# Optimization experiments

Measured on AMD Instinct MI355X. Metric: run time of the kernel, lower is better.

## Reference

```python
import jax, jax.numpy as jnp
import numpy as np

N_NODES = 100000
N_EDGES = 1250000
D_IN = 64
D_H = 64
D_OUT = 32


def setup_inputs() -> dict:
    key = jax.random.key(0)
    ks = jax.random.split(key, 8)
    x = jax.random.normal(ks[0], (N_NODES, D_IN), dtype=jnp.float32)
    edge_index = jax.random.randint(ks[1], (2, N_EDGES), 0, N_NODES, dtype=jnp.int64)
    s = 0.1
    W1_l = jax.random.normal(ks[2], (D_H, D_IN), dtype=jnp.float32) * s
    W1_r = jax.random.normal(ks[3], (D_H, D_IN), dtype=jnp.float32) * s
    b1 = jnp.zeros((D_H,), dtype=jnp.float32)
    W2_l = jax.random.normal(ks[4], (D_OUT, D_H), dtype=jnp.float32) * s
    W2_r = jax.random.normal(ks[5], (D_OUT, D_H), dtype=jnp.float32) * s
    b2 = jnp.zeros((D_OUT,), dtype=jnp.float32)
    return {"x": x, "edge_index": edge_index, "W1_l": W1_l, "W1_r": W1_r,
            "b1": b1, "W2_l": W2_l, "W2_r": W2_r, "b2": b2}


def _sage_conv(x, src, dst, W_l, W_r, b):
    # PyG SAGEConv (aggr='mean', root_weight=True):
    #   out = lin_l(mean_{j in N(i)} x_j) + lin_r(x_i)
    n = x.shape[0]
    msg = x[src]                                            # [E, d] gather
    ssum = jax.ops.segment_sum(msg, dst, num_segments=n)    # [N, d]
    deg = jax.ops.segment_sum(jnp.ones((src.shape[0], 1), x.dtype), dst,
                              num_segments=n)               # [N, 1]
    mean = ssum / jnp.maximum(deg, 1.0)
    return mean @ W_l.T + b + x @ W_r.T


def reference(x, edge_index, W1_l, W1_r, b1, W2_l, W2_r, b2):
    src = edge_index[0]
    dst = edge_index[1]
    h = jax.nn.relu(_sage_conv(x, src, dst, W1_l, W1_r, b1))
    out = _sage_conv(h, src, dst, W2_l, W2_r, b2)
    return out
```

## Files before the change

kernel.cpp:

```cpp
#include <hip/hip_runtime.h>

#define N_NODES 100000
#define N_EDGES 1250000
#define D_IN 64
#define D_H 64
#define D_OUT 32

#define BUCKETS 196
#define GRP 512
#define PREP_NB 512
#define PREP_CH 2442
#define SCAP 48
#define BSTRIDE (PREP_NB*SCAP)
#define CSRCAP 8192

typedef __attribute__((ext_vector_type(8))) short bf16x8;
typedef __attribute__((ext_vector_type(4))) float f32x4;

__device__ __forceinline__ unsigned short f2bf(float f) {
    unsigned u = __float_as_uint(f);
    u = (u + 0x7fffu + ((u >> 16) & 1u)) >> 16;
    return (unsigned short)u;
}
__device__ __forceinline__ float bfhi(unsigned v) { return __uint_as_float(v & 0xffff0000u); }
__device__ __forceinline__ float bflo(unsigned v) { return __uint_as_float(v << 16); }


__global__ __launch_bounds__(256) void k_prep(const float* __restrict__ x,
                                              unsigned short* __restrict__ xh,
                                              const int* __restrict__ src,
                                              const int* __restrict__ dst,
                                              int* __restrict__ ebuf,
                                              int* __restrict__ pcnt) {
    __shared__ int ofs[BUCKETS];
    int t = threadIdx.x, b = blockIdx.x;
    for (int i = t; i < BUCKETS; i += 256) ofs[i] = 0;
    __syncthreads();

    const int TOT = N_NODES * 64 / 4;
    for (int i = b * 256 + t; i < TOT; i += PREP_NB * 256) {
        float4 v = *(const float4*)(x + (size_t)i * 4);
        uint2 u;
        u.x = (unsigned)f2bf(v.x) | ((unsigned)f2bf(v.y) << 16);
        u.y = (unsigned)f2bf(v.z) | ((unsigned)f2bf(v.w) << 16);
        *(uint2*)(xh + (size_t)i * 4) = u;
    }

    int e0 = b * PREP_CH;
    int e1 = e0 + PREP_CH; if (e1 > N_EDGES) e1 = N_EDGES;
    for (int e = e0 + t; e < e1; e += 256) {
        int s = src[e], d = dst[e];
        if ((unsigned)d >= N_NODES) continue;
        int sv = ((unsigned)s < N_NODES) ? s : 0;
        int bk = d >> 9;
        int r = atomicAdd(&ofs[bk], 1);
        if (r < SCAP) ebuf[bk * BSTRIDE + b * SCAP + r] = ((d & 511) << 17) | sv;
    }
    __syncthreads();
    for (int i = t; i < BUCKETS; i += 256) {
        int v = ofs[i]; if (v > SCAP) v = SCAP;
        pcnt[b * BUCKETS + i] = v;
    }
}

__global__ __launch_bounds__(256) void k_phb(const int* __restrict__ ebuf,
                                             const int* __restrict__ pcnt,
                                             int2* __restrict__ rd,
                                             int* __restrict__ csr_src) {
    __shared__ int sedge[CSRCAP];
    __shared__ int pc[PREP_NB];
    __shared__ int cnt[GRP];
    __shared__ int part[256];
    int b = blockIdx.x, t = threadIdx.x;

    int c0 = pcnt[(2 * t) * BUCKETS + b];
    int c1 = pcnt[(2 * t + 1) * BUCKETS + b];
    int s = c0 + c1;
    part[t] = s;
    __syncthreads();
    for (int off = 1; off < 256; off <<= 1) {
        int u = (t >= off) ? part[t - off] : 0;
        __syncthreads();
        part[t] += u;
        __syncthreads();
    }
    int run = part[t] - s;
    pc[2 * t] = run;
    pc[2 * t + 1] = run + c0;
    int n = part[255]; if (n > CSRCAP) n = CSRCAP;
    for (int i = t; i < GRP; i += 256) cnt[i] = 0;
    {
        const int* sp = ebuf + b * BSTRIDE + (2 * t) * SCAP;
        int base = pc[2 * t];
        for (int j = 0; j < c0; ++j) if (base + j < CSRCAP) sedge[base + j] = sp[j];
        sp += SCAP;
        base = pc[2 * t + 1];
        for (int j = 0; j < c1; ++j) if (base + j < CSRCAP) sedge[base + j] = sp[j];
    }
    __syncthreads();
    for (int i = t; i < n; i += 256) atomicAdd(&cnt[sedge[i] >> 17], 1);
    __syncthreads();
    int d0 = cnt[2 * t], d1 = cnt[2 * t + 1];
    int s2 = d0 + d1;
    part[t] = s2;
    __syncthreads();
    for (int off = 1; off < 256; off <<= 1) {
        int u = (t >= off) ? part[t - off] : 0;
        __syncthreads();
        part[t] += u;
        __syncthreads();
    }
    int g0 = b * CSRCAP + part[t] - s2;
    int node0 = b * GRP + 2 * t;
    if (node0 + 1 < N_NODES) {
        *(int4*)(rd + node0) = make_int4(g0, d0, g0 + d0, d1);
    } else if (node0 < N_NODES) {
        rd[node0] = make_int2(g0, d0);
    }
    __syncthreads();
    cnt[2 * t] = g0;
    cnt[2 * t + 1] = g0 + d0;
    __syncthreads();
    for (int i = t; i < n; i += 256) {
        int v = sedge[i];
        int pos = atomicAdd(&cnt[v >> 17], 1);
        csr_src[pos] = v & 0x1FFFF;
    }
}

__global__ __launch_bounds__(256) void k_gather1(
    const unsigned short* __restrict__ xh,
    const int2* __restrict__ rd,
    const int* __restrict__ csr_src,
    unsigned int* __restrict__ meanh)
{
    int lane = threadIdx.x & 63;
    int wv = threadIdx.x >> 6;
    int c = lane & 31;
    int hb = lane & 32;
    const unsigned* xp = (const unsigned*)xh;

    int node0 = blockIdx.x * 8 + wv * 2 + (hb >> 5);
    for (int row = node0; row < N_NODES; row += gridDim.x * 8) {
        int2 rdv = rd[row];
        int start = rdv.x, dg = rdv.y;
        int end = start + dg;
        float x0 = 0.f, y0 = 0.f, x1 = 0.f, y1 = 0.f;
        float x2 = 0.f, y2 = 0.f, x3 = 0.f, y3 = 0.f;
        float x4 = 0.f, y4 = 0.f, x5 = 0.f, y5 = 0.f;
        float x6 = 0.f, y6 = 0.f, x7 = 0.f, y7 = 0.f;
        for (int eb = start; eb < end; eb += 32) {
            int nv = end - eb; if (nv > 32) nv = 32;
            int sid = (c < nv) ? csr_src[eb + c] : 0;
            int j = 0;
            for (; j + 8 <= nv; j += 8) {
                int s0 = __shfl(sid, hb + j + 0, 64);
                int s1 = __shfl(sid, hb + j + 1, 64);
                int s2 = __shfl(sid, hb + j + 2, 64);
                int s3 = __shfl(sid, hb + j + 3, 64);
                int s4 = __shfl(sid, hb + j + 4, 64);
                int s5 = __shfl(sid, hb + j + 5, 64);
                int s6 = __shfl(sid, hb + j + 6, 64);
                int s7 = __shfl(sid, hb + j + 7, 64);
                unsigned v0 = xp[s0 * 32 + c];
                unsigned v1 = xp[s1 * 32 + c];
                unsigned v2 = xp[s2 * 32 + c];
                unsigned v3 = xp[s3 * 32 + c];
                unsigned v4 = xp[s4 * 32 + c];
                unsigned v5 = xp[s5 * 32 + c];
                unsigned v6 = xp[s6 * 32 + c];
                unsigned v7 = xp[s7 * 32 + c];
                x0 += bflo(v0); y0 += bfhi(v0);
                x1 += bflo(v1); y1 += bfhi(v1);
                x2 += bflo(v2); y2 += bfhi(v2);
                x3 += bflo(v3); y3 += bfhi(v3);
                x4 += bflo(v4); y4 += bfhi(v4);
                x5 += bflo(v5); y5 += bfhi(v5);
                x6 += bflo(v6); y6 += bfhi(v6);
                x7 += bflo(v7); y7 += bfhi(v7);
            }
            for (; j + 4 <= nv; j += 4) {
                int s0 = __shfl(sid, hb + j + 0, 64);
                int s1 = __shfl(sid, hb + j + 1, 64);
                int s2 = __shfl(sid, hb + j + 2, 64);
                int s3 = __shfl(sid, hb + j + 3, 64);
                unsigned v0 = xp[s0 * 32 + c];
                unsigned v1 = xp[s1 * 32 + c];
                unsigned v2 = xp[s2 * 32 + c];
                unsigned v3 = xp[s3 * 32 + c];
                x0 += bflo(v0); y0 += bfhi(v0);
                x1 += bflo(v1); y1 += bfhi(v1);
                x2 += bflo(v2); y2 += bfhi(v2);
                x3 += bflo(v3); y3 += bfhi(v3);
            }
            for (; j < nv; ++j) {
                int s = __shfl(sid, hb + j, 64);
                unsigned v = xp[s * 32 + c];
                x0 += bflo(v); y0 += bfhi(v);
            }
        }
        float rdeg = 1.0f / fmaxf((float)dg, 1.0f);
        float fx = (((x0 + x1) + (x2 + x3)) + ((x4 + x5) + (x6 + x7))) * rdeg;
        float fy = (((y0 + y1) + (y2 + y3)) + ((y4 + y5) + (y6 + y7))) * rdeg;
        meanh[(size_t)row * 32 + c] = (unsigned)f2bf(fx) | ((unsigned)f2bf(fy) << 16);
    }
}

__global__ __launch_bounds__(256) void k_gemm1(
    const unsigned short* __restrict__ xh, const unsigned short* __restrict__ meanh,
    const float* __restrict__ W1l, const float* __restrict__ W1r,
    const float* __restrict__ b1,
    const float* __restrict__ W2l, const float* __restrict__ W2r,
    unsigned short* __restrict__ hWlh, unsigned short* __restrict__ hrh)
{
    __shared__ short sWB1[4 * 4 * 64 * 8];
    __shared__ short sWB2[2 * 4 * 64 * 8];
    __shared__ short htile[4][16 * 72];

    int tid = threadIdx.x;
    for (int e = tid; e < 1024; e += 256) {
        int kc = e >> 8, nt = (e >> 6) & 3, ln = e & 63;
        int cc = ln & 15, qd = ln >> 4;
        int n = nt * 16 + cc, k0 = kc * 32 + qd * 8;
        const float* sp = (k0 < 64) ? (W1l + n * 64 + k0) : (W1r + n * 64 + (k0 - 64));
        short* dp = sWB1 + e * 8;
        #pragma unroll
        for (int j = 0; j < 8; ++j) dp[j] = (short)f2bf(sp[j]);
    }
    for (int e = tid; e < 512; e += 256) {
        int kc = e >> 8, nt = (e >> 6) & 3, ln = e & 63;
        int cc = ln & 15, qd = ln >> 4;
        int n = nt * 16 + cc, k0 = kc * 32 + qd * 8;
        const float* sp = (n < 32) ? (W2l + n * 64 + k0) : (W2r + (n - 32) * 64 + k0);
        short* dp = sWB2 + e * 8;
        #pragma unroll
        for (int j = 0; j < 8; ++j) dp[j] = (short)f2bf(sp[j]);
    }
    __syncthreads();

    int lane = tid & 63, w = tid >> 6;
    int c = lane & 15, quad = lane >> 4;
    float bias[4];
    #pragma unroll
    for (int nt = 0; nt < 4; ++nt) bias[nt] = b1[nt * 16 + c];

    const bf16x8* B1 = (const bf16x8*)sWB1;
    const bf16x8* B2 = (const bf16x8*)sWB2;
    short* ht = htile[w];

    for (int r0 = blockIdx.x * 64 + w * 16; r0 < N_NODES; r0 += gridDim.x * 64) {
        int ra = r0 + c; if (ra > N_NODES - 1) ra = N_NODES - 1;
        const bf16x8* mrow = (const bf16x8*)(meanh + (size_t)ra * 64);
        const bf16x8* xrow = (const bf16x8*)(xh + (size_t)ra * 64);
        bf16x8 a0 = mrow[quad];
        bf16x8 a1 = mrow[4 + quad];
        bf16x8 a2 = xrow[quad];
        bf16x8 a3 = xrow[4 + quad];

        f32x4 acc[4];
        #pragma unroll
        for (int nt = 0; nt < 4; ++nt) acc[nt] = (f32x4){0.f, 0.f, 0.f, 0.f};
        #pragma unroll
        for (int nt = 0; nt < 4; ++nt)
            acc[nt] = __builtin_amdgcn_mfma_f32_16x16x32_bf16(a0, B1[(0 * 4 + nt) * 64 + lane], acc[nt], 0, 0, 0);
        #pragma unroll
        for (int nt = 0; nt < 4; ++nt)
            acc[nt] = __builtin_amdgcn_mfma_f32_16x16x32_bf16(a1, B1[(1 * 4 + nt) * 64 + lane], acc[nt], 0, 0, 0);
        #pragma unroll
        for (int nt = 0; nt < 4; ++nt)
            acc[nt] = __builtin_amdgcn_mfma_f32_16x16x32_bf16(a2, B1[(2 * 4 + nt) * 64 + lane], acc[nt], 0, 0, 0);
        #pragma unroll
        for (int nt = 0; nt < 4; ++nt)
            acc[nt] = __builtin_amdgcn_mfma_f32_16x16x32_bf16(a3, B1[(3 * 4 + nt) * 64 + lane], acc[nt], 0, 0, 0);

        #pragma unroll
        for (int nt = 0; nt < 4; ++nt) {
            #pragma unroll
            for (int reg = 0; reg < 4; ++reg) {
                float hv = fmaxf(acc[nt][reg] + bias[nt], 0.0f);
                ht[(quad * 4 + reg) * 72 + nt * 16 + c] = (short)f2bf(hv);
            }
        }
        bf16x8 h0 = *(const bf16x8*)(ht + c * 72 + 0  + quad * 8);
        bf16x8 h1 = *(const bf16x8*)(ht + c * 72 + 32 + quad * 8);

        f32x4 acc2[4];
        #pragma unroll
        for (int nt = 0; nt < 4; ++nt) acc2[nt] = (f32x4){0.f, 0.f, 0.f, 0.f};
        #pragma unroll
        for (int nt = 0; nt < 4; ++nt)
            acc2[nt] = __builtin_amdgcn_mfma_f32_16x16x32_bf16(h0, B2[(0 * 4 + nt) * 64 + lane], acc2[nt], 0, 0, 0);
        #pragma unroll
        for (int nt = 0; nt < 4; ++nt)
            acc2[nt] = __builtin_amdgcn_mfma_f32_16x16x32_bf16(h1, B2[(1 * 4 + nt) * 64 + lane], acc2[nt], 0, 0, 0);

        #pragma unroll
        for (int nt = 0; nt < 4; ++nt) {
            #pragma unroll
            for (int reg = 0; reg < 4; ++reg) {
                int row = r0 + quad * 4 + reg;
                if (row < N_NODES) {
                    unsigned short q = f2bf(acc2[nt][reg]);
                    if (nt < 2) hWlh[(size_t)row * 32 + nt * 16 + c] = q;
                    else        hrh [(size_t)row * 32 + (nt - 2) * 16 + c] = q;
                }
            }
        }
    }
}

__global__ __launch_bounds__(256) void k_l2(
    const unsigned short* __restrict__ hWlh, const unsigned short* __restrict__ hrh,
    const int2* __restrict__ rd,
    const int* __restrict__ csr_src,
    const float* __restrict__ b2, float* __restrict__ out)
{
    int lane = threadIdx.x & 63;
    int wv = threadIdx.x >> 6;
    int c = lane & 15;
    int qb = lane & 48;
    const unsigned* hp  = (const unsigned*)hWlh;
    const unsigned* hrp = (const unsigned*)hrh;
    float2 b2v = ((const float2*)b2)[c];

    int node0 = blockIdx.x * 16 + wv * 4 + (qb >> 4);
    for (int row = node0; row < N_NODES; row += gridDim.x * 16) {
        int2 rdv = rd[row];
        int start = rdv.x, dg = rdv.y;
        int end = start + dg;
        float x0 = 0.f, y0 = 0.f, x1 = 0.f, y1 = 0.f;
        float x2 = 0.f, y2 = 0.f, x3 = 0.f, y3 = 0.f;
        float x4 = 0.f, y4 = 0.f, x5 = 0.f, y5 = 0.f;
        float x6 = 0.f, y6 = 0.f, x7 = 0.f, y7 = 0.f;
        for (int eb = start; eb < end; eb += 16) {
            int nv = end - eb; if (nv > 16) nv = 16;
            int sid = (c < nv) ? csr_src[eb + c] : 0;
            int j = 0;
            for (; j + 8 <= nv; j += 8) {
                int s0 = __shfl(sid, qb + j + 0, 64);
                int s1 = __shfl(sid, qb + j + 1, 64);
                int s2 = __shfl(sid, qb + j + 2, 64);
                int s3 = __shfl(sid, qb + j + 3, 64);
                int s4 = __shfl(sid, qb + j + 4, 64);
                int s5 = __shfl(sid, qb + j + 5, 64);
                int s6 = __shfl(sid, qb + j + 6, 64);
                int s7 = __shfl(sid, qb + j + 7, 64);
                unsigned v0 = hp[s0 * 16 + c];
                unsigned v1 = hp[s1 * 16 + c];
                unsigned v2 = hp[s2 * 16 + c];
                unsigned v3 = hp[s3 * 16 + c];
                unsigned v4 = hp[s4 * 16 + c];
                unsigned v5 = hp[s5 * 16 + c];
                unsigned v6 = hp[s6 * 16 + c];
                unsigned v7 = hp[s7 * 16 + c];
                x0 += bflo(v0); y0 += bfhi(v0);
                x1 += bflo(v1); y1 += bfhi(v1);
                x2 += bflo(v2); y2 += bfhi(v2);
                x3 += bflo(v3); y3 += bfhi(v3);
                x4 += bflo(v4); y4 += bfhi(v4);
                x5 += bflo(v5); y5 += bfhi(v5);
                x6 += bflo(v6); y6 += bfhi(v6);
                x7 += bflo(v7); y7 += bfhi(v7);
            }
            for (; j + 4 <= nv; j += 4) {
                int s0 = __shfl(sid, qb + j + 0, 64);
                int s1 = __shfl(sid, qb + j + 1, 64);
                int s2 = __shfl(sid, qb + j + 2, 64);
                int s3 = __shfl(sid, qb + j + 3, 64);
                unsigned v0 = hp[s0 * 16 + c];
                unsigned v1 = hp[s1 * 16 + c];
                unsigned v2 = hp[s2 * 16 + c];
                unsigned v3 = hp[s3 * 16 + c];
                x0 += bflo(v0); y0 += bfhi(v0);
                x1 += bflo(v1); y1 += bfhi(v1);
                x2 += bflo(v2); y2 += bfhi(v2);
                x3 += bflo(v3); y3 += bfhi(v3);
            }
            for (; j < nv; ++j) {
                int s = __shfl(sid, qb + j, 64);
                unsigned v = hp[s * 16 + c];
                x0 += bflo(v); y0 += bfhi(v);
            }
        }
        float fx = ((x0 + x1) + (x2 + x3)) + ((x4 + x5) + (x6 + x7));
        float fy = ((y0 + y1) + (y2 + y3)) + ((y4 + y5) + (y6 + y7));
        float rdeg = 1.0f / fmaxf((float)dg, 1.0f);
        unsigned hru = hrp[(size_t)row * 16 + c];
        float2 o;
        o.x = fmaf(fx, rdeg, bflo(hru) + b2v.x);
        o.y = fmaf(fy, rdeg, bfhi(hru) + b2v.y);
        ((float2*)out)[(size_t)row * 16 + c] = o;
    }
}

extern "C" void kernel_launch(void* const* d_in, const int* in_sizes, int n_in,
                              void* d_out, int out_size, void* d_ws, size_t ws_size,
                              hipStream_t stream) {
    const float* x   = (const float*)d_in[0];
    const int*   ei  = (const int*)d_in[1];
    const float* W1l = (const float*)d_in[2];
    const float* W1r = (const float*)d_in[3];
    const float* b1  = (const float*)d_in[4];
    const float* W2l = (const float*)d_in[5];
    const float* W2r = (const float*)d_in[6];
    const float* b2  = (const float*)d_in[7];
    float* out = (float*)d_out;

    const int* src = ei;
    const int* dst = ei + N_EDGES;

    char* w = (char*)d_ws;
    int2* rd     = (int2*)w;  w += sizeof(int2) * (N_NODES + 4);
    int* pcnt    = (int*)w;   w += sizeof(int) * (PREP_NB * BUCKETS);
    int* csr_src = (int*)w;   w += sizeof(int) * (BUCKETS * CSRCAP);
    int* ebuf    = (int*)w;   w += sizeof(int) * ((size_t)BUCKETS * BSTRIDE);
    unsigned short* xh    = (unsigned short*)w; w += sizeof(short) * (size_t)N_NODES * 64;
    unsigned int*   meanh = (unsigned int*)w;   w += sizeof(int)   * (size_t)N_NODES * 32;
    unsigned short* hWlh  = (unsigned short*)w; w += sizeof(short) * (size_t)N_NODES * 32;
    unsigned short* hrh   = (unsigned short*)w;

    k_prep<<<PREP_NB, 256, 0, stream>>>(x, xh, src, dst, ebuf, pcnt);
    k_phb<<<BUCKETS, 256, 0, stream>>>(ebuf, pcnt, rd, csr_src);
    k_gather1<<<4096, 256, 0, stream>>>(xh, rd, csr_src, meanh);
    k_gemm1<<<(N_NODES + 63) / 64, 256, 0, stream>>>(
        xh, (const unsigned short*)meanh, W1l, W1r, b1, W2l, W2r, hWlh, hrh);
    k_l2<<<4096, 256, 0, stream>>>(hWlh, hrh, rd, csr_src, b2, out);
}
```

Baseline: 199.8 us.

## Rework CSR bucket kernel with wave-shuffle scans and 512-thread blocks

The per-bucket CSR build kernel now runs 512 threads, one per source block and one per node. The Hillis-Steele shared-memory scans, which needed many barriers, become wavefront __shfl_up scans plus a small cross-wave sum. The pcnt layout is transposed so each bucket's counts are read contiguously, and edge staging uses int4 loads. The goal is fewer barriers and better coalescing in a small latency-bound kernel. The gain is limited to one of five kernels.

```diff
diff --git a/kernel.cpp b/kernel.cpp
--- a/kernel.cpp
+++ b/kernel.cpp
@@ -59,69 +59,70 @@
     __syncthreads();
     for (int i = t; i < BUCKETS; i += 256) {
         int v = ofs[i]; if (v > SCAP) v = SCAP;
-        pcnt[b * BUCKETS + i] = v;
-    }
-}
-
-__global__ __launch_bounds__(256) void k_phb(const int* __restrict__ ebuf,
+        pcnt[i * PREP_NB + b] = v;
+    }
+}
+
+__global__ __launch_bounds__(512) void k_phb(const int* __restrict__ ebuf,
                                              const int* __restrict__ pcnt,
                                              int2* __restrict__ rd,
                                              int* __restrict__ csr_src) {
     __shared__ int sedge[CSRCAP];
-    __shared__ int pc[PREP_NB];
     __shared__ int cnt[GRP];
-    __shared__ int part[256];
+    __shared__ int wsum[8];
     int b = blockIdx.x, t = threadIdx.x;
-
-    int c0 = pcnt[(2 * t) * BUCKETS + b];
-    int c1 = pcnt[(2 * t + 1) * BUCKETS + b];
-    int s = c0 + c1;
-    part[t] = s;
-    __syncthreads();
-    for (int off = 1; off < 256; off <<= 1) {
-        int u = (t >= off) ? part[t - off] : 0;
-        __syncthreads();
-        part[t] += u;
-        __syncthreads();
-    }
-    int run = part[t] - s;
-    pc[2 * t] = run;
-    pc[2 * t + 1] = run + c0;
-    int n = part[255]; if (n > CSRCAP) n = CSRCAP;
-    for (int i = t; i < GRP; i += 256) cnt[i] = 0;
+    int lane = t & 63, w = t >> 6;
+
+    cnt[t] = 0;
+    int c = pcnt[b * PREP_NB + t];
+
+    int run = c;
+    #pragma unroll
+    for (int off = 1; off < 64; off <<= 1) {
+        int u = __shfl_up(run, off, 64);
+        if (lane >= off) run += u;
+    }
+    if (lane == 63) wsum[w] = run;
+    __syncthreads();
+    int wbase = 0, tot = 0;
+    #pragma unroll
+    for (int i = 0; i < 8; ++i) { int v = wsum[i]; tot += v; if (i < w) wbase += v; }
+    int base = wbase + run - c;
+    int n = tot; if (n > CSRCAP) n = CSRCAP;
+
     {
-        const int* sp = ebuf + b * BSTRIDE + (2 * t) * SCAP;
-        int base = pc[2 * t];
-        for (int j = 0; j < c0; ++j) if (base + j < CSRCAP) sedge[base + j] = sp[j];
-        sp += SCAP;
-        base = pc[2 * t + 1];
-        for (int j = 0; j < c1; ++j) if (base + j < CSRCAP) sedge[base + j] = sp[j];
-    }
-    __syncthreads();
-    for (int i = t; i < n; i += 256) atomicAdd(&cnt[sedge[i] >> 17], 1);
-    __syncthreads();
-    int d0 = cnt[2 * t], d1 = cnt[2 * t + 1];
-    int s2 = d0 + d1;
-    part[t] = s2;
-    __syncthreads();
-    for (int off = 1; off < 256; off <<= 1) {
-        int u = (t >= off) ? part[t - off] : 0;
-        __syncthreads();
-        part[t] += u;
-        __syncthreads();
-    }
-    int g0 = b * CSRCAP + part[t] - s2;
-    int node0 = b * GRP + 2 * t;
-    if (node0 + 1 < N_NODES) {
-        *(int4*)(rd + node0) = make_int4(g0, d0, g0 + d0, d1);
-    } else if (node0 < N_NODES) {
-        rd[node0] = make_int2(g0, d0);
-    }
-    __syncthreads();
-    cnt[2 * t] = g0;
-    cnt[2 * t + 1] = g0 + d0;
-    __syncthreads();
-    for (int i = t; i < n; i += 256) {
+        const int4* sp4 = (const int4*)(ebuf + (size_t)b * BSTRIDE + (size_t)t * SCAP);
+        for (int j = 0; j < c; j += 4) {
+            int4 v = sp4[j >> 2];
+            int p = base + j;
+            if (p + 0 < CSRCAP)          sedge[p + 0] = v.x;
+            if (j + 1 < c && p + 1 < CSRCAP) sedge[p + 1] = v.y;
+            if (j + 2 < c && p + 2 < CSRCAP) sedge[p + 2] = v.z;
+            if (j + 3 < c && p + 3 < CSRCAP) sedge[p + 3] = v.w;
+        }
+    }
+    __syncthreads();
+    for (int i = t; i < n; i += 512) atomicAdd(&cnt[sedge[i] >> 17], 1);
+    __syncthreads();
+
+    int d = cnt[t];
+    int rund = d;
+    #pragma unroll
+    for (int off = 1; off < 64; off <<= 1) {
+        int u = __shfl_up(rund, off, 64);
+        if (lane >= off) rund += u;
+    }
+    if (lane == 63) wsum[w] = rund;
+    __syncthreads();
+    int wb2 = 0;
+    #pragma unroll
+    for (int i = 0; i < 8; ++i) { if (i < w) wb2 += wsum[i]; }
+    int gabs = b * CSRCAP + wb2 + rund - d;
+    int node = b * GRP + t;
+    if (node < N_NODES) rd[node] = make_int2(gabs, d);
+    cnt[t] = gabs;
+    __syncthreads();
+    for (int i = t; i < n; i += 512) {
         int v = sedge[i];
         int pos = atomicAdd(&cnt[v >> 17], 1);
         csr_src[pos] = v & 0x1FFFF;
@@ -420,7 +421,7 @@
     unsigned short* hrh   = (unsigned short*)w;
 
     k_prep<<<PREP_NB, 256, 0, stream>>>(x, xh, src, dst, ebuf, pcnt);
-    k_phb<<<BUCKETS, 256, 0, stream>>>(ebuf, pcnt, rd, csr_src);
+    k_phb<<<BUCKETS, 512, 0, stream>>>(ebuf, pcnt, rd, csr_src);
     k_gather1<<<4096, 256, 0, stream>>>(xh, rd, csr_src, meanh);
     k_gemm1<<<(N_NODES + 63) / 64, 256, 0, stream>>>(
         xh, (const unsigned short*)meanh, W1l, W1r, b1, W2l, W2r, hWlh, hrh);
```

Result: faster. 195.7 us (-2.1%).
